# Kernel tuning notes

Measured on AMD Instinct MI355X. Metric: run time of the kernel, lower is better.

The kernel has to match this reference:

```python
import jax, jax.numpy as jnp
import numpy as np

EPS = 1e-6

def _mlp3(x, Wa, ba, Wb, bb, Wc, bc):
    h = jax.nn.relu(x @ Wa + ba)
    h = jax.nn.relu(h @ Wb + bb)
    return h @ Wc + bc

def setup_inputs() -> dict:
    key = jax.random.key(0)
    ks = jax.random.split(key, 16)
    B, D, C, N = 1024, 1024, 128, 100000
    s = 0.02  # weight scale
    return {
        "query": jax.random.normal(ks[0], (B, D), jnp.float32),
        "W1": jax.random.normal(ks[1], (D, D // 2), jnp.float32) * s,
        "b1": jnp.zeros((D // 2,), jnp.float32),
        "W2": jax.random.normal(ks[2], (D // 2, D // 4), jnp.float32) * s,
        "b2": jnp.zeros((D // 4,), jnp.float32),
        "W3": jax.random.normal(ks[3], (D // 4, C), jnp.float32) * s,
        "b3": jnp.zeros((C,), jnp.float32),
        "keys": jax.random.normal(ks[4], (N, C), jnp.float32),
        "values": jax.random.normal(ks[5], (N, C), jnp.float32),
        "D1w": jax.random.normal(ks[6], (C, D // 4), jnp.float32) * s,
        "D1b": jnp.zeros((D // 4,), jnp.float32),
        "D2w": jax.random.normal(ks[7], (D // 4, D // 2), jnp.float32) * s,
        "D2b": jnp.zeros((D // 2,), jnp.float32),
        "D3w": jax.random.normal(ks[8], (D // 2, D), jnp.float32) * s,
        "D3b": jnp.zeros((D,), jnp.float32),
        "k": 5,
    }

def reference(query, W1, b1, W2, b2, W3, b3, keys, values,
              D1w, D1b, D2w, D2b, D3w, D3b, k):
    # Compress query (FAISS path detaches, so stop_gradient is faithful)
    cq = _mlp3(query, W1, b1, W2, b2, W3, b3)          # [B, C]
    cq = jax.lax.stop_gradient(cq)
    keys_c = jax.lax.stop_gradient(keys)
    vals = jax.lax.stop_gradient(values)               # stored values were .detach()ed
    # Brute-force squared-L2 distances (IndexFlatL2 returns squared L2): [B, N]
    d2 = (jnp.sum(cq * cq, axis=1, keepdims=True)
          + jnp.sum(keys_c * keys_c, axis=1)[None, :]
          - 2.0 * cq @ keys_c.T)
    neg_d, idx = jax.lax.top_k(-d2, k)                 # k nearest, ascending distance
    dist = -neg_d                                      # [B, k]
    w = 1.0 / (dist + EPS)
    w = w / jnp.sum(w, axis=1, keepdims=True)          # [B, k]
    gathered = vals[idx]                               # [B, k, C]
    weighted = jnp.einsum('bk,bkc->bc', w, gathered)   # [B, C]
    retrieved = _mlp3(weighted, D1w, D1b, D2w, D2b, D3w, D3b)  # [B, D]
    confidence = 1.0 / (dist[:, 0] + EPS)              # [B]
    return retrieved, confidence
```

## Files before the change

### kernel.cpp

```cpp
#include <hip/hip_runtime.h>
#include <hip/hip_bf16.h>

#define NKEYS  100000
#define NCH    128
#define CHK    832
#define TPC    13
#define KPAD   (NCH * CHK)
#define NTILE  (KPAD / 64)
#define BQ     1024
#define EPS_F  1e-6f
#define NCAND  (NCH * 3)
#define BIGF   1e30f

typedef __attribute__((ext_vector_type(8))) short bf16x8;
typedef __attribute__((ext_vector_type(4))) float f32x4;

__device__ __forceinline__ void gl_lds16(const uint4* g, uint4* l) {
    __builtin_amdgcn_global_load_lds((const __attribute__((address_space(1))) void*)g,
                                     (__attribute__((address_space(3))) void*)l, 16, 0, 0);
}
__device__ __forceinline__ unsigned umn(unsigned a, unsigned b) { return a < b ? a : b; }
__device__ __forceinline__ unsigned umx(unsigned a, unsigned b) { return a > b ? a : b; }
__device__ __forceinline__ ushort bf16bits(float v) {
    __hip_bfloat16 h = __float2bfloat16(v);
    return *(ushort*)&h;
}

__device__ __forceinline__ void ins3u(unsigned (&m)[3], unsigned u) {
    unsigned v1 = umn(m[2], u);
    m[2] = umx(m[1], v1);
    unsigned v2 = umn(m[1], v1);
    m[1] = umx(m[0], v2);
    m[0] = umn(m[0], v2);
}

__device__ __forceinline__ void ins5(float (&d)[5], int (&ix)[5], float nd, int ni) {
    if (nd < d[4]) {
        d[4] = nd; ix[4] = ni;
#pragma unroll
        for (int p = 4; p > 0; --p) {
            if (d[p] < d[p - 1]) {
                float td = d[p]; d[p] = d[p - 1]; d[p - 1] = td;
                int   ti = ix[p]; ix[p] = ix[p - 1]; ix[p - 1] = ti;
            }
        }
    }
}

__global__ __launch_bounds__(256)
void cvt_keys(const float* __restrict__ keys, uint4* __restrict__ img,
              float* __restrict__ kk, float* __restrict__ khalf) {
    const int tid = threadIdx.x;
    const int r = tid >> 2, s = tid & 3;
    const int tile = blockIdx.x;
    const int n = tile * 64 + r;
    const int ct = r >> 4, l15 = r & 15;
    const bool live = (n < NKEYS);
    const float* kp = keys + (size_t)n * 128 + s * 32;
    float ss = 0.f;
    uint4 out[4];
#pragma unroll
    for (int q = 0; q < 4; ++q) {
        float4 a = make_float4(0.f, 0.f, 0.f, 0.f), b = a;
        if (live) { a = *(const float4*)(kp + q * 8); b = *(const float4*)(kp + q * 8 + 4); }
        ss += a.x * a.x + a.y * a.y + a.z * a.z + a.w * a.w
            + b.x * b.x + b.y * b.y + b.z * b.z + b.w * b.w;
        float v[8] = {a.x, a.y, a.z, a.w, b.x, b.y, b.z, b.w};
        ushort h[8];
#pragma unroll
        for (int j = 0; j < 8; ++j) h[j] = bf16bits(v[j]);
        out[q] = make_uint4((uint)h[0] | ((uint)h[1] << 16), (uint)h[2] | ((uint)h[3] << 16),
                            (uint)h[4] | ((uint)h[5] << 16), (uint)h[6] | ((uint)h[7] << 16));
    }
    ss += __shfl_xor(ss, 1, 64);
    ss += __shfl_xor(ss, 2, 64);
    if (s == 0) {
        kk[n]    = live ? ss : BIGF;
        khalf[n] = live ? -0.5f * ss : -BIGF;
    }
#pragma unroll
    for (int q = 0; q < 4; ++q)
        img[(size_t)tile * 1024 + ((ct * 4 + s) * 4 + q) * 16 + l15] = out[q];
}

__global__ __launch_bounds__(256)
void sgemm_part(const float* __restrict__ A, const float* __restrict__ W,
                float* __restrict__ P, int M, int N, int K, int kslice) {
    __shared__ float As[16][68];
    __shared__ float Bs[16][64];
    const int tid = threadIdx.x;
    const int tx = tid & 15, ty = tid >> 4;
    const int m0 = blockIdx.y * 64, n0 = blockIdx.x * 64;
    const int kb = blockIdx.z * kslice, ke = kb + kslice;
    float acc[4][4] = {};
    for (int k0 = kb; k0 < ke; k0 += 16) {
        {
            int m = tid >> 2, k4 = (tid & 3) * 4;
            float4 a = *(const float4*)&A[(size_t)(m0 + m) * K + k0 + k4];
            As[k4 + 0][m] = a.x; As[k4 + 1][m] = a.y;
            As[k4 + 2][m] = a.z; As[k4 + 3][m] = a.w;
        }
        {
            int k = tid >> 4, n4 = (tid & 15) * 4;
            *(float4*)&Bs[k][n4] = *(const float4*)&W[(size_t)(k0 + k) * N + n0 + n4];
        }
        __syncthreads();
#pragma unroll
        for (int kkk = 0; kkk < 16; ++kkk) {
            float4 a4 = *(const float4*)&As[kkk][ty * 4];
            float4 b4 = *(const float4*)&Bs[kkk][tx * 4];
            float av[4] = {a4.x, a4.y, a4.z, a4.w};
            float bv[4] = {b4.x, b4.y, b4.z, b4.w};
#pragma unroll
            for (int i = 0; i < 4; ++i)
#pragma unroll
                for (int j = 0; j < 4; ++j)
                    acc[i][j] = fmaf(av[i], bv[j], acc[i][j]);
        }
        __syncthreads();
    }
    P += (size_t)blockIdx.z * M * N;
#pragma unroll
    for (int i = 0; i < 4; ++i)
        *(float4*)&P[(size_t)(m0 + ty * 4 + i) * N + n0 + tx * 4] =
            make_float4(acc[i][0], acc[i][1], acc[i][2], acc[i][3]);
}

template <int RELU>
__global__ __launch_bounds__(256)
void reduce_bias(const float* __restrict__ P, const float* __restrict__ bias,
                 float* __restrict__ C, int MN, int N, int nP) {
    int i4 = (blockIdx.x * 256 + threadIdx.x) * 4;
    if (i4 >= MN) return;
    float4 s = *(const float4*)&P[i4];
    for (int p = 1; p < nP; ++p) {
        float4 v = *(const float4*)&P[(size_t)p * MN + i4];
        s.x += v.x; s.y += v.y; s.z += v.z; s.w += v.w;
    }
    float4 b = *(const float4*)&bias[i4 % N];
    s.x += b.x; s.y += b.y; s.z += b.z; s.w += b.w;
    if (RELU) {
        s.x = fmaxf(s.x, 0.f); s.y = fmaxf(s.y, 0.f);
        s.z = fmaxf(s.z, 0.f); s.w = fmaxf(s.w, 0.f);
    }
    *(float4*)&C[i4] = s;
}

__global__ __launch_bounds__(256)
void rowsq128(const float* __restrict__ X, float* __restrict__ out, int nrows) {
    int lane = threadIdx.x & 63;
    int row  = blockIdx.x * 4 + (threadIdx.x >> 6);
    if (row >= nrows) return;
    const float* x = X + (size_t)row * 128;
    float a = x[lane], b = x[lane + 64];
    float v = a * a + b * b;
#pragma unroll
    for (int off = 32; off > 0; off >>= 1) v += __shfl_down(v, off, 64);
    if (lane == 0) out[row] = v;
}

__global__ __launch_bounds__(256)
void cvt_bf16_rne(const float* __restrict__ in, ushort* __restrict__ out, int n) {
    int i = (blockIdx.x * 256 + threadIdx.x) * 4;
    if (i >= n) return;
    float4 v = *(const float4*)&in[i];
    ushort4 o;
    o.x = bf16bits(v.x); o.y = bf16bits(v.y); o.z = bf16bits(v.z); o.w = bf16bits(v.w);
    *(ushort4*)&out[i] = o;
}

__global__ __launch_bounds__(256)
void cvt_wT(const float* __restrict__ W, uint4* __restrict__ Wimg, int K, int N) {
    const int ctile = blockIdx.x, p = blockIdx.y;
    const int npan = K >> 6;
#pragma unroll
    for (int it = 0; it < 2; ++it) {
        int c = it * 256 + threadIdx.x;
        int l15 = c & 15, quad = (c >> 4) & 3, s = (c >> 6) & 1, ct = c >> 7;
        int n = ctile * 64 + ct * 16 + l15;
        int k = p * 64 + s * 32 + quad * 8;
        ushort h[8];
#pragma unroll
        for (int j = 0; j < 8; ++j) h[j] = bf16bits(W[(size_t)(k + j) * N + n]);
        Wimg[((size_t)ctile * npan + p) * 512 + c] =
            make_uint4((uint)h[0] | ((uint)h[1] << 16), (uint)h[2] | ((uint)h[3] << 16),
                       (uint)h[4] | ((uint)h[5] << 16), (uint)h[6] | ((uint)h[7] << 16));
    }
}

__global__ __launch_bounds__(512, 4)
void screen_topk(const ushort* __restrict__ qbf, const uint4* __restrict__ img,
                 const float* __restrict__ khalf, int* __restrict__ cand_i) {
    __shared__ uint4 buf[2][1024];
    __shared__ float kls[CHK];
    const int tid = threadIdx.x;
    const int wv = tid >> 6, ln = tid & 63;
    const int quad = ln >> 4, l15 = ln & 15;
    const int m0 = blockIdx.y * 256 + wv * 32;
    const int c0 = blockIdx.x * CHK;
    const int t0 = blockIdx.x * TPC;

    bf16x8 afA[4], afB[4];
    {
        const ushort* qa = qbf + (size_t)(m0 + l15) * 128 + quad * 8;
#pragma unroll
        for (int s = 0; s < 4; ++s) {
            afA[s] = *(const bf16x8*)(qa + 32 * s);
            afB[s] = *(const bf16x8*)(qa + 16 * 128 + 32 * s);
        }
    }
    for (int i = tid; i < CHK; i += 512) kls[i] = khalf[c0 + i];

    unsigned mA[4][3], mB[4][3];
#pragma unroll
    for (int r = 0; r < 4; ++r)
#pragma unroll
        for (int p = 0; p < 3; ++p) { mA[r][p] = 0xFFFFFFFFu; mB[r][p] = 0xFFFFFFFFu; }

#pragma unroll
    for (int it = 0; it < 2; ++it)
        gl_lds16(&img[(size_t)t0 * 1024 + it * 512 + wv * 64 + ln],
                 &buf[0][it * 512 + wv * 64]);
    __syncthreads();

    for (int t = 0; t < TPC; ++t) {
        const int b = t & 1;
        if (t + 1 < TPC) {
#pragma unroll
            for (int it = 0; it < 2; ++it)
                gl_lds16(&img[(size_t)(t0 + t + 1) * 1024 + it * 512 + wv * 64 + ln],
                         &buf[b ^ 1][it * 512 + wv * 64]);
        }
#pragma unroll
        for (int ct = 0; ct < 4; ++ct) {
            const int nl = t * 64 + ct * 16 + l15;
            const float kh = kls[nl];
            f32x4 a0 = {kh, kh, kh, kh}, a1 = {kh, kh, kh, kh};
#pragma unroll
            for (int s = 0; s < 4; ++s) {
                bf16x8 bfr = *(const bf16x8*)&buf[b][(ct * 4 + s) * 64 + ln];
                a0 = __builtin_amdgcn_mfma_f32_16x16x32_bf16(afA[s], bfr, a0, 0, 0, 0);
                a1 = __builtin_amdgcn_mfma_f32_16x16x32_bf16(afB[s], bfr, a1, 0, 0, 0);
            }
#pragma unroll
            for (int r = 0; r < 4; ++r) {
                ins3u(mA[r], (__float_as_uint(a0[r]) & 0xFFFFF800u) | (unsigned)nl);
                ins3u(mB[r], (__float_as_uint(a1[r]) & 0xFFFFF800u) | (unsigned)nl);
            }
        }
        __syncthreads();
    }

#pragma unroll
    for (int set = 0; set < 2; ++set) {
#pragma unroll
        for (int r = 0; r < 4; ++r) {
            unsigned m[3];
#pragma unroll
            for (int p = 0; p < 3; ++p) m[p] = set ? mB[r][p] : mA[r][p];
#pragma unroll
            for (int st = 1; st <= 8; st <<= 1) {
                unsigned o[3];
#pragma unroll
                for (int p = 0; p < 3; ++p) o[p] = (unsigned)__shfl_xor((int)m[p], st, 64);
#pragma unroll
                for (int p = 0; p < 3; ++p) ins3u(m, o[p]);
            }
            if (l15 == 0) {
                const int row = m0 + set * 16 + quad * 4 + r;
#pragma unroll
                for (int p = 0; p < 3; ++p)
                    cand_i[((size_t)row * NCH + blockIdx.x) * 3 + p] = c0 + (int)(m[p] & 0x7FFu);
            }
        }
    }
}

__global__ __launch_bounds__(512)
void rerank_gather(const int* __restrict__ cand_i, const float* __restrict__ cq,
                   const float* __restrict__ keysf, const float* __restrict__ qq,
                   const float* __restrict__ kk, const float* __restrict__ values,
                   ushort* __restrict__ wbf, float* __restrict__ conf_out) {
    __shared__ __align__(16) float qs[128];
    __shared__ float ed[NCAND];
    __shared__ int   ei[NCAND];
    __shared__ float w5[5];
    __shared__ int   s5[5];
    __shared__ float confs;
    const int row = blockIdx.x, tid = threadIdx.x;
    const int ln = tid & 63;
    const int qd = tid >> 4;
    const int l15 = tid & 15;
    if (tid < 128) qs[tid] = cq[(size_t)row * 128 + tid];
    for (int c = tid; c < NCAND; c += 512) ei[c] = cand_i[(size_t)row * NCAND + c];
    __syncthreads();
    const float4 qa = *(const float4*)&qs[l15 * 8];
    const float4 qb = *(const float4*)&qs[l15 * 8 + 4];
    const float qqr = qq[row];
#pragma unroll 3
    for (int it = 0; it < (NCAND + 31) / 32; ++it) {
        const int c = qd + it * 32;
        if (c < NCAND) {
            const int idx = ei[c];
            const int idc = idx < NKEYS ? idx : NKEYS - 1;
            const float* kp = &keysf[(size_t)idc * 128 + l15 * 8];
            const float4 ka = *(const float4*)kp;
            const float4 kb = *(const float4*)(kp + 4);
            float dot = qa.x * ka.x + qa.y * ka.y + qa.z * ka.z + qa.w * ka.w
                      + qb.x * kb.x + qb.y * kb.y + qb.z * kb.z + qb.w * kb.w;
            dot += __shfl_xor(dot, 1, 64);
            dot += __shfl_xor(dot, 2, 64);
            dot += __shfl_xor(dot, 4, 64);
            dot += __shfl_xor(dot, 8, 64);
            if (l15 == 0) ed[c] = qqr + kk[idx] - 2.0f * dot;
        }
    }
    __syncthreads();
    if (tid < 64) {
        float bd[5]; int bi[5];
#pragma unroll
        for (int p = 0; p < 5; ++p) { bd[p] = BIGF; bi[p] = 0; }
        for (int c = ln; c < NCAND; c += 64) ins5(bd, bi, ed[c], ei[c]);
#pragma unroll
        for (int m = 1; m <= 32; m <<= 1) {
            float od[5]; int oi[5];
#pragma unroll
            for (int p = 0; p < 5; ++p) {
                od[p] = __shfl_xor(bd[p], m, 64);
                oi[p] = __shfl_xor(bi[p], m, 64);
            }
#pragma unroll
            for (int p = 0; p < 5; ++p) ins5(bd, bi, od[p], oi[p]);
        }
        if (ln == 0) {
            float ww[5]; float s = 0.f;
#pragma unroll
            for (int p = 0; p < 5; ++p) { ww[p] = 1.0f / (bd[p] + EPS_F); s += ww[p]; }
#pragma unroll
            for (int p = 0; p < 5; ++p) { w5[p] = ww[p] / s; s5[p] = bi[p]; }
            confs = 1.0f / (bd[0] + EPS_F);
        }
    }
    __syncthreads();
    if (tid < 128) {
        float acc = 0.f;
#pragma unroll
        for (int p = 0; p < 5; ++p) acc += w5[p] * values[(size_t)s5[p] * 128 + tid];
        wbf[(size_t)row * 128 + tid] = bf16bits(acc);
    }
    if (tid == 0) conf_out[row] = confs;
}

template <int RELU, int OUTF32>
__global__ __launch_bounds__(256)
void bgemm_bias(const ushort* __restrict__ Abf, const uint4* __restrict__ Wimg,
                const float* __restrict__ bias, void* __restrict__ Cout,
                int M, int N, int K) {
    __shared__ uint4 pan[2][512];
    const int tid = threadIdx.x;
    const int wv = tid >> 6, ln = tid & 63;
    const int quad = ln >> 4, l15 = ln & 15;
    const int n0 = blockIdx.x * 64;
    const int m0 = blockIdx.y * 128 + wv * 32;
    const int ctile = blockIdx.x, npan = K >> 6;
    f32x4 acc[2][4];
#pragma unroll
    for (int s = 0; s < 2; ++s)
#pragma unroll
        for (int c = 0; c < 4; ++c) acc[s][c] = (f32x4){0.f, 0.f, 0.f, 0.f};

#pragma unroll
    for (int it = 0; it < 2; ++it)
        gl_lds16(&Wimg[(size_t)ctile * npan * 512 + it * 256 + wv * 64 + ln],
                 &pan[0][it * 256 + wv * 64]);
    __syncthreads();

    for (int p = 0; p < npan; ++p) {
        const int b = p & 1;
        if (p + 1 < npan) {
#pragma unroll
            for (int it = 0; it < 2; ++it)
                gl_lds16(&Wimg[((size_t)ctile * npan + p + 1) * 512 + it * 256 + wv * 64 + ln],
                         &pan[b ^ 1][it * 256 + wv * 64]);
        }
        const ushort* arow = Abf + (size_t)(m0 + l15) * K + p * 64 + quad * 8;
        bf16x8 afA[2], afB[2];
#pragma unroll
        for (int s = 0; s < 2; ++s) {
            afA[s] = *(const bf16x8*)(arow + s * 32);
            afB[s] = *(const bf16x8*)(arow + (size_t)16 * K + s * 32);
        }
#pragma unroll
        for (int ct = 0; ct < 4; ++ct)
#pragma unroll
            for (int s = 0; s < 2; ++s) {
                bf16x8 bfr = *(const bf16x8*)&pan[b][((ct * 2 + s) * 4 + quad) * 16 + l15];
                acc[0][ct] = __builtin_amdgcn_mfma_f32_16x16x32_bf16(afA[s], bfr, acc[0][ct], 0, 0, 0);
                acc[1][ct] = __builtin_amdgcn_mfma_f32_16x16x32_bf16(afB[s], bfr, acc[1][ct], 0, 0, 0);
            }
        __syncthreads();
    }

#pragma unroll
    for (int ct = 0; ct < 4; ++ct) {
        const int col = n0 + ct * 16 + l15;
        const float bv = bias[col];
#pragma unroll
        for (int set = 0; set < 2; ++set)
#pragma unroll
            for (int r = 0; r < 4; ++r) {
                float v = acc[set][ct][r] + bv;
                if (RELU) v = fmaxf(v, 0.f);
                const int row = m0 + set * 16 + quad * 4 + r;
                if (OUTF32) {
                    ((float*)Cout)[(size_t)row * N + col] = v;
                } else {
                    ((ushort*)Cout)[(size_t)row * N + col] = bf16bits(v);
                }
            }
    }
}

extern "C" void kernel_launch(void* const* d_in, const int* in_sizes, int n_in,
                              void* d_out, int out_size, void* d_ws, size_t ws_size,
                              hipStream_t stream) {
    const float* query  = (const float*)d_in[0];
    const float* W1     = (const float*)d_in[1];
    const float* b1     = (const float*)d_in[2];
    const float* W2     = (const float*)d_in[3];
    const float* b2     = (const float*)d_in[4];
    const float* W3     = (const float*)d_in[5];
    const float* b3     = (const float*)d_in[6];
    const float* keys   = (const float*)d_in[7];
    const float* values = (const float*)d_in[8];
    const float* D1w    = (const float*)d_in[9];
    const float* D1b    = (const float*)d_in[10];
    const float* D2w    = (const float*)d_in[11];
    const float* D2b    = (const float*)d_in[12];
    const float* D3w    = (const float*)d_in[13];
    const float* D3b    = (const float*)d_in[14];
    float* out = (float*)d_out;

    float*  ws    = (float*)d_ws;
    float*  kk    = ws;
    float*  khalf = ws + 106496;
    float*  qq    = ws + 212992;
    float*  cq    = ws + 214016;
    ushort* qbf   = (ushort*)(ws + 345088);
    int*    cand  = (int*)(ws + 410624);
    float*  R     = ws + 803840;
    float*  part  = R;
    float*  h1    = R + 2097152;
    float*  h2    = R + 2621440;
    uint4*  img   = (uint4*)R;
    ushort* wbf   = (ushort*)R;
    ushort* h3bf  = (ushort*)(R + 65536);
    ushort* h4bf  = (ushort*)(R + 196608);
    uint4*  Wimg1 = (uint4*)(R + 458752);
    uint4*  Wimg2 = (uint4*)(R + 475136);
    uint4*  Wimg3 = (uint4*)(R + 540672);
    float*  conf  = out + 1024 * 1024;

    sgemm_part<<<dim3(8, 16, 4), 256, 0, stream>>>(query, W1, part, 1024, 512, 1024, 256);
    reduce_bias<1><<<512, 256, 0, stream>>>(part, b1, h1, 1024 * 512, 512, 4);
    sgemm_part<<<dim3(4, 16, 8), 256, 0, stream>>>(h1, W2, part, 1024, 256, 512, 64);
    reduce_bias<1><<<256, 256, 0, stream>>>(part, b2, h2, 1024 * 256, 256, 8);
    sgemm_part<<<dim3(2, 16, 8), 256, 0, stream>>>(h2, W3, part, 1024, 128, 256, 32);
    reduce_bias<0><<<128, 256, 0, stream>>>(part, b3, cq, 1024 * 128, 128, 8);
    rowsq128<<<256, 256, 0, stream>>>(cq, qq, BQ);
    cvt_bf16_rne<<<128, 256, 0, stream>>>(cq, qbf, BQ * 128);
    cvt_keys<<<NTILE, 256, 0, stream>>>(keys, img, kk, khalf);
    screen_topk<<<dim3(NCH, BQ / 256), 512, 0, stream>>>(qbf, img, khalf, cand);
    rerank_gather<<<BQ, 512, 0, stream>>>(cand, cq, keys, qq, kk, values, wbf, conf);
    cvt_wT<<<dim3(4, 2),  256, 0, stream>>>(D1w, Wimg1, 128, 256);
    cvt_wT<<<dim3(8, 4),  256, 0, stream>>>(D2w, Wimg2, 256, 512);
    cvt_wT<<<dim3(16, 8), 256, 0, stream>>>(D3w, Wimg3, 512, 1024);
    bgemm_bias<1, 0><<<dim3(4, 8),  256, 0, stream>>>(wbf,  Wimg1, D1b, h3bf, 1024, 256,  128);
    bgemm_bias<1, 0><<<dim3(8, 8),  256, 0, stream>>>(h3bf, Wimg2, D2b, h4bf, 1024, 512,  256);
    bgemm_bias<0, 1><<<dim3(16, 8), 256, 0, stream>>>(h4bf, Wimg3, D3b, out,  1024, 1024, 512);

    (void)in_sizes; (void)n_in; (void)out_size; (void)ws_size;
}
```

Measured before the change: 298.4 us.

## Run first encoder GEMM on bf16x3 split MFMA and fuse split-K reductions

The first encoder layer (1024x1024x512) moves from the fp32 SIMT sgemm to bf16 MFMA. Each operand is split into high and low bf16 parts and three products are accumulated along a tripled K, keeping accuracy close to fp32. The separate reduce_bias kernels are removed: each following sgemm sums the previous split-K partials, adds bias and applies ReLU while loading A, and a final_row kernel merges the last reduction with the bf16 conversion and row-norm computation. The three decoder weight conversions are merged into one launch. This cuts launches and intermediate traffic, but adds split/conversion passes and a larger partials buffer, and the next sgemm rereads partials redundantly across its column blocks.

```diff
diff --git a/kernel.cpp b/kernel.cpp
--- a/kernel.cpp
+++ b/kernel.cpp
@@ -84,8 +84,119 @@
 }
 
 __global__ __launch_bounds__(256)
-void sgemm_part(const float* __restrict__ A, const float* __restrict__ W,
-                float* __restrict__ P, int M, int N, int K, int kslice) {
+void split_a(const float* __restrict__ A, ushort* __restrict__ Ax, int K) {
+    const int row = blockIdx.x;
+    for (int i = threadIdx.x * 4; i < K; i += 1024) {
+        float4 v = *(const float4*)&A[(size_t)row * K + i];
+        float x[4] = {v.x, v.y, v.z, v.w};
+        ushort h[4], l[4];
+#pragma unroll
+        for (int j = 0; j < 4; ++j) {
+            __hip_bfloat16 hb = __float2bfloat16(x[j]);
+            h[j] = *(ushort*)&hb;
+            l[j] = bf16bits(x[j] - __bfloat162float(hb));
+        }
+        ushort* o = Ax + (size_t)row * 3 * K;
+        *(ushort4*)&o[i]         = make_ushort4(h[0], h[1], h[2], h[3]);
+        *(ushort4*)&o[K + i]     = make_ushort4(l[0], l[1], l[2], l[3]);
+        *(ushort4*)&o[2 * K + i] = make_ushort4(h[0], h[1], h[2], h[3]);
+    }
+}
+
+__global__ __launch_bounds__(256)
+void cvt_wT_split(const float* __restrict__ W, uint4* __restrict__ Wimg,
+                  int Ksrc, int N) {
+    const int ctile = blockIdx.x, p = blockIdx.y;
+    const int npanT = gridDim.y;
+    const int pk = Ksrc >> 6;
+    const int part = p / pk, psrc = p - part * pk;
+#pragma unroll
+    for (int it = 0; it < 2; ++it) {
+        int c = it * 256 + threadIdx.x;
+        int l15 = c & 15, quad = (c >> 4) & 3, s = (c >> 6) & 1, ct = c >> 7;
+        int n = ctile * 64 + ct * 16 + l15;
+        int k = psrc * 64 + s * 32 + quad * 8;
+        ushort h[8];
+#pragma unroll
+        for (int j = 0; j < 8; ++j) {
+            float w = W[(size_t)(k + j) * N + n];
+            __hip_bfloat16 hb = __float2bfloat16(w);
+            if (part < 2) h[j] = *(ushort*)&hb;
+            else h[j] = bf16bits(w - __bfloat162float(hb));
+        }
+        Wimg[((size_t)ctile * npanT + p) * 512 + c] =
+            make_uint4((uint)h[0] | ((uint)h[1] << 16), (uint)h[2] | ((uint)h[3] << 16),
+                       (uint)h[4] | ((uint)h[5] << 16), (uint)h[6] | ((uint)h[7] << 16));
+    }
+}
+
+__global__ __launch_bounds__(256)
+void bgemm_part(const ushort* __restrict__ Abf, const uint4* __restrict__ Wimg,
+                float* __restrict__ P, int M, int N, int K, int ppz) {
+    __shared__ uint4 pan[2][512];
+    const int tid = threadIdx.x;
+    const int wv = tid >> 6, ln = tid & 63;
+    const int quad = ln >> 4, l15 = ln & 15;
+    const int n0 = blockIdx.x * 64;
+    const int m0 = blockIdx.y * 128 + wv * 32;
+    const int ctile = blockIdx.x, npanT = K >> 6;
+    const int p0 = blockIdx.z * ppz;
+    f32x4 acc[2][4];
+#pragma unroll
+    for (int s = 0; s < 2; ++s)
+#pragma unroll
+        for (int c = 0; c < 4; ++c) acc[s][c] = (f32x4){0.f, 0.f, 0.f, 0.f};
+
+#pragma unroll
+    for (int it = 0; it < 2; ++it)
+        gl_lds16(&Wimg[((size_t)ctile * npanT + p0) * 512 + it * 256 + wv * 64 + ln],
+                 &pan[0][it * 256 + wv * 64]);
+    __syncthreads();
+
+    for (int pp = 0; pp < ppz; ++pp) {
+        const int p = p0 + pp;
+        const int b = pp & 1;
+        if (pp + 1 < ppz) {
+#pragma unroll
+            for (int it = 0; it < 2; ++it)
+                gl_lds16(&Wimg[((size_t)ctile * npanT + p + 1) * 512 + it * 256 + wv * 64 + ln],
+                         &pan[b ^ 1][it * 256 + wv * 64]);
+        }
+        const ushort* arow = Abf + (size_t)(m0 + l15) * K + p * 64 + quad * 8;
+        bf16x8 afA[2], afB[2];
+#pragma unroll
+        for (int s = 0; s < 2; ++s) {
+            afA[s] = *(const bf16x8*)(arow + s * 32);
+            afB[s] = *(const bf16x8*)(arow + (size_t)16 * K + s * 32);
+        }
+#pragma unroll
+        for (int ct = 0; ct < 4; ++ct)
+#pragma unroll
+            for (int s = 0; s < 2; ++s) {
+                bf16x8 bfr = *(const bf16x8*)&pan[b][((ct * 2 + s) * 4 + quad) * 16 + l15];
+                acc[0][ct] = __builtin_amdgcn_mfma_f32_16x16x32_bf16(afA[s], bfr, acc[0][ct], 0, 0, 0);
+                acc[1][ct] = __builtin_amdgcn_mfma_f32_16x16x32_bf16(afB[s], bfr, acc[1][ct], 0, 0, 0);
+            }
+        __syncthreads();
+    }
+
+    P += (size_t)blockIdx.z * M * N;
+#pragma unroll
+    for (int ct = 0; ct < 4; ++ct) {
+        const int col = n0 + ct * 16 + l15;
+#pragma unroll
+        for (int set = 0; set < 2; ++set)
+#pragma unroll
+            for (int r = 0; r < 4; ++r)
+                P[(size_t)(m0 + set * 16 + quad * 4 + r) * N + col] = acc[set][ct][r];
+    }
+}
+
+template <int NP>
+__global__ __launch_bounds__(256)
+void sgemm_part(const float* __restrict__ A, const float* __restrict__ abias,
+                const float* __restrict__ W, float* __restrict__ P,
+                int M, int N, int K, int kslice, int MNpart) {
     __shared__ float As[16][68];
     __shared__ float Bs[16][64];
     const int tid = threadIdx.x;
@@ -96,7 +207,18 @@
     for (int k0 = kb; k0 < ke; k0 += 16) {
         {
             int m = tid >> 2, k4 = (tid & 3) * 4;
-            float4 a = *(const float4*)&A[(size_t)(m0 + m) * K + k0 + k4];
+            const float* ap = &A[(size_t)(m0 + m) * K + k0 + k4];
+            float4 a = *(const float4*)ap;
+            if (NP > 0) {
+#pragma unroll
+                for (int z = 1; z < NP; ++z) {
+                    float4 v = *(const float4*)(ap + (size_t)z * MNpart);
+                    a.x += v.x; a.y += v.y; a.z += v.z; a.w += v.w;
+                }
+                float4 b = *(const float4*)&abias[k0 + k4];
+                a.x = fmaxf(a.x + b.x, 0.f); a.y = fmaxf(a.y + b.y, 0.f);
+                a.z = fmaxf(a.z + b.z, 0.f); a.w = fmaxf(a.w + b.w, 0.f);
+            }
             As[k4 + 0][m] = a.x; As[k4 + 1][m] = a.y;
             As[k4 + 2][m] = a.z; As[k4 + 3][m] = a.w;
         }
@@ -126,52 +248,28 @@
             make_float4(acc[i][0], acc[i][1], acc[i][2], acc[i][3]);
 }
 
-template <int RELU>
-__global__ __launch_bounds__(256)
-void reduce_bias(const float* __restrict__ P, const float* __restrict__ bias,
-                 float* __restrict__ C, int MN, int N, int nP) {
-    int i4 = (blockIdx.x * 256 + threadIdx.x) * 4;
-    if (i4 >= MN) return;
-    float4 s = *(const float4*)&P[i4];
-    for (int p = 1; p < nP; ++p) {
-        float4 v = *(const float4*)&P[(size_t)p * MN + i4];
-        s.x += v.x; s.y += v.y; s.z += v.z; s.w += v.w;
-    }
-    float4 b = *(const float4*)&bias[i4 % N];
-    s.x += b.x; s.y += b.y; s.z += b.z; s.w += b.w;
-    if (RELU) {
-        s.x = fmaxf(s.x, 0.f); s.y = fmaxf(s.y, 0.f);
-        s.z = fmaxf(s.z, 0.f); s.w = fmaxf(s.w, 0.f);
-    }
-    *(float4*)&C[i4] = s;
-}
-
-__global__ __launch_bounds__(256)
-void rowsq128(const float* __restrict__ X, float* __restrict__ out, int nrows) {
-    int lane = threadIdx.x & 63;
-    int row  = blockIdx.x * 4 + (threadIdx.x >> 6);
-    if (row >= nrows) return;
-    const float* x = X + (size_t)row * 128;
-    float a = x[lane], b = x[lane + 64];
-    float v = a * a + b * b;
-#pragma unroll
-    for (int off = 32; off > 0; off >>= 1) v += __shfl_down(v, off, 64);
-    if (lane == 0) out[row] = v;
-}
-
-__global__ __launch_bounds__(256)
-void cvt_bf16_rne(const float* __restrict__ in, ushort* __restrict__ out, int n) {
-    int i = (blockIdx.x * 256 + threadIdx.x) * 4;
-    if (i >= n) return;
-    float4 v = *(const float4*)&in[i];
-    ushort4 o;
-    o.x = bf16bits(v.x); o.y = bf16bits(v.y); o.z = bf16bits(v.z); o.w = bf16bits(v.w);
-    *(ushort4*)&out[i] = o;
-}
-
-__global__ __launch_bounds__(256)
-void cvt_wT(const float* __restrict__ W, uint4* __restrict__ Wimg, int K, int N) {
-    const int ctile = blockIdx.x, p = blockIdx.y;
+__global__ __launch_bounds__(128)
+void final_row(const float* __restrict__ P, const float* __restrict__ bias,
+               float* __restrict__ cq, ushort* __restrict__ qbf,
+               float* __restrict__ qq) {
+    __shared__ float red[2];
+    const int row = blockIdx.x, c = threadIdx.x;
+    float v = 0.f;
+#pragma unroll
+    for (int z = 0; z < 8; ++z) v += P[(size_t)z * (BQ * 128) + row * 128 + c];
+    v += bias[c];
+    cq[(size_t)row * 128 + c] = v;
+    qbf[(size_t)row * 128 + c] = bf16bits(v);
+    float s = v * v;
+#pragma unroll
+    for (int off = 32; off > 0; off >>= 1) s += __shfl_down(s, off, 64);
+    if ((c & 63) == 0) red[c >> 6] = s;
+    __syncthreads();
+    if (c == 0) qq[row] = red[0] + red[1];
+}
+
+__device__ __forceinline__ void wT_panel(const float* __restrict__ W, uint4* __restrict__ Wimg,
+                                         int K, int N, int ctile, int p) {
     const int npan = K >> 6;
 #pragma unroll
     for (int it = 0; it < 2; ++it) {
@@ -186,6 +284,16 @@
             make_uint4((uint)h[0] | ((uint)h[1] << 16), (uint)h[2] | ((uint)h[3] << 16),
                        (uint)h[4] | ((uint)h[5] << 16), (uint)h[6] | ((uint)h[7] << 16));
     }
+}
+
+__global__ __launch_bounds__(256)
+void cvt_wT_all(const float* __restrict__ W1, const float* __restrict__ W2,
+                const float* __restrict__ W3, uint4* __restrict__ I1,
+                uint4* __restrict__ I2, uint4* __restrict__ I3) {
+    int b = blockIdx.x;
+    if (b < 8)       { wT_panel(W1, I1, 128, 256,  b >> 1, b & 1); }
+    else if (b < 40) { b -= 8;  wT_panel(W2, I2, 256, 512,  b >> 2, b & 3); }
+    else             { b -= 40; wT_panel(W3, I3, 512, 1024, b >> 3, b & 7); }
 }
 
 __global__ __launch_bounds__(512, 4)
@@ -412,11 +520,8 @@
                 float v = acc[set][ct][r] + bv;
                 if (RELU) v = fmaxf(v, 0.f);
                 const int row = m0 + set * 16 + quad * 4 + r;
-                if (OUTF32) {
-                    ((float*)Cout)[(size_t)row * N + col] = v;
-                } else {
-                    ((ushort*)Cout)[(size_t)row * N + col] = bf16bits(v);
-                }
+                if (OUTF32) ((float*)Cout)[(size_t)row * N + col] = v;
+                else        ((ushort*)Cout)[(size_t)row * N + col] = bf16bits(v);
             }
     }
 }
@@ -449,9 +554,11 @@
     ushort* qbf   = (ushort*)(ws + 345088);
     int*    cand  = (int*)(ws + 410624);
     float*  R     = ws + 803840;
-    float*  part  = R;
-    float*  h1    = R + 2097152;
-    float*  h2    = R + 2621440;
+    ushort* xbig  = (ushort*)R;
+    uint4*  W1img = (uint4*)(R + 1572864);
+    float*  partA = R + 2359296;
+    float*  partB = R + 5505024;
+    float*  partC = R + 7602176;
     uint4*  img   = (uint4*)R;
     ushort* wbf   = (ushort*)R;
     ushort* h3bf  = (ushort*)(R + 65536);
@@ -461,20 +568,16 @@
     uint4*  Wimg3 = (uint4*)(R + 540672);
     float*  conf  = out + 1024 * 1024;
 
-    sgemm_part<<<dim3(8, 16, 4), 256, 0, stream>>>(query, W1, part, 1024, 512, 1024, 256);
-    reduce_bias<1><<<512, 256, 0, stream>>>(part, b1, h1, 1024 * 512, 512, 4);
-    sgemm_part<<<dim3(4, 16, 8), 256, 0, stream>>>(h1, W2, part, 1024, 256, 512, 64);
-    reduce_bias<1><<<256, 256, 0, stream>>>(part, b2, h2, 1024 * 256, 256, 8);
-    sgemm_part<<<dim3(2, 16, 8), 256, 0, stream>>>(h2, W3, part, 1024, 128, 256, 32);
-    reduce_bias<0><<<128, 256, 0, stream>>>(part, b3, cq, 1024 * 128, 128, 8);
-    rowsq128<<<256, 256, 0, stream>>>(cq, qq, BQ);
-    cvt_bf16_rne<<<128, 256, 0, stream>>>(cq, qbf, BQ * 128);
+    split_a<<<1024, 256, 0, stream>>>(query, xbig, 1024);
+    cvt_wT_split<<<dim3(8, 48), 256, 0, stream>>>(W1, W1img, 1024, 512);
+    bgemm_part<<<dim3(8, 8, 6), 256, 0, stream>>>(xbig, W1img, partA, 1024, 512, 3072, 8);
+    sgemm_part<6><<<dim3(4, 16, 8), 256, 0, stream>>>(partA, b1, W2, partB, 1024, 256, 512, 64, 1024 * 512);
+    sgemm_part<8><<<dim3(2, 16, 8), 256, 0, stream>>>(partB, b2, W3, partC, 1024, 128, 256, 32, 1024 * 256);
+    final_row<<<1024, 128, 0, stream>>>(partC, b3, cq, qbf, qq);
     cvt_keys<<<NTILE, 256, 0, stream>>>(keys, img, kk, khalf);
     screen_topk<<<dim3(NCH, BQ / 256), 512, 0, stream>>>(qbf, img, khalf, cand);
     rerank_gather<<<BQ, 512, 0, stream>>>(cand, cq, keys, qq, kk, values, wbf, conf);
-    cvt_wT<<<dim3(4, 2),  256, 0, stream>>>(D1w, Wimg1, 128, 256);
-    cvt_wT<<<dim3(8, 4),  256, 0, stream>>>(D2w, Wimg2, 256, 512);
-    cvt_wT<<<dim3(16, 8), 256, 0, stream>>>(D3w, Wimg3, 512, 1024);
+    cvt_wT_all<<<168, 256, 0, stream>>>(D1w, D2w, D3w, Wimg1, Wimg2, Wimg3);
     bgemm_bias<1, 0><<<dim3(4, 8),  256, 0, stream>>>(wbf,  Wimg1, D1b, h3bf, 1024, 256,  128);
     bgemm_bias<1, 0><<<dim3(8, 8),  256, 0, stream>>>(h3bf, Wimg2, D2b, h4bf, 1024, 512,  256);
     bgemm_bias<0, 1><<<dim3(16, 8), 256, 0, stream>>>(h4bf, Wimg3, D3b, out,  1024, 1024, 512);
```

Measured after the change: 284.1 us. 4.8% less time.
